# Kernel optimization log

Hardware: AMD Instinct MI355X
Metric: run time of the kernel (lower is better)

## Reference

```python
import jax, jax.numpy as jnp
import numpy as np

HEADS = 8
DIM_HEAD = 96
INNER = HEADS * DIM_HEAD  # 768
PEP_DIM = 768
PRO_DIM = 768
SCALE = DIM_HEAD ** -0.5
NEG = -1000000.0
EPS = 1e-5


def _layer_norm(x, g, b):
    mu = jnp.mean(x, axis=-1, keepdims=True)
    var = jnp.mean(jnp.square(x - mu), axis=-1, keepdims=True)
    return (x - mu) * jax.lax.rsqrt(var + EPS) * g + b


def setup_inputs() -> dict:
    key = jax.random.key(0)
    ks = jax.random.split(key, 12)
    b, n, m = 16, 128, 2048
    peptide = jax.random.normal(ks[0], (b, n, PEP_DIM), dtype=jnp.float32)
    protein = jax.random.normal(ks[1], (b, m, PRO_DIM), dtype=jnp.float32)
    peptide_mask = jax.random.randint(ks[2], (b, n), 0, 2, dtype=jnp.int32)
    pro_mask = jax.random.randint(ks[3], (b, m), 0, 2, dtype=jnp.int32)
    s = 0.02
    Wq = jax.random.normal(ks[4], (PEP_DIM, INNER), dtype=jnp.float32) * s
    Wk = jax.random.normal(ks[5], (PRO_DIM, INNER), dtype=jnp.float32) * s
    Wv_prot = jax.random.normal(ks[6], (PRO_DIM, INNER), dtype=jnp.float32) * s
    Wv_pep = jax.random.normal(ks[7], (PEP_DIM, INNER), dtype=jnp.float32) * s
    Wo_prot = jax.random.normal(ks[8], (INNER, PEP_DIM), dtype=jnp.float32) * s
    bo_prot = jnp.zeros((PEP_DIM,), dtype=jnp.float32)
    Wo_pep = jax.random.normal(ks[9], (INNER, PRO_DIM), dtype=jnp.float32) * s
    bo_pep = jnp.zeros((PRO_DIM,), dtype=jnp.float32)
    ln_g = jnp.ones((PEP_DIM,), dtype=jnp.float32)
    ln_b = jnp.zeros((PEP_DIM,), dtype=jnp.float32)
    return {
        'peptide': peptide, 'protein': protein,
        'peptide_mask': peptide_mask, 'pro_mask': pro_mask,
        'Wq': Wq, 'Wk': Wk, 'Wv_prot': Wv_prot, 'Wv_pep': Wv_pep,
        'Wo_prot': Wo_prot, 'bo_prot': bo_prot,
        'Wo_pep': Wo_pep, 'bo_pep': bo_pep,
        'ln_g': ln_g, 'ln_b': ln_b,
    }


def reference(peptide, protein, peptide_mask, pro_mask,
              Wq, Wk, Wv_prot, Wv_pep, Wo_prot, bo_prot, Wo_pep, bo_pep,
              ln_g, ln_b):
    b, n, _ = peptide.shape
    m = protein.shape[1]
    # projections -> (b, h, len, d)
    q = (peptide @ Wq).reshape(b, n, HEADS, DIM_HEAD).transpose(0, 2, 1, 3)
    k = (protein @ Wk).reshape(b, m, HEADS, DIM_HEAD).transpose(0, 2, 1, 3)
    v_prot = (protein @ Wv_prot).reshape(b, m, HEADS, DIM_HEAD).transpose(0, 2, 1, 3)
    v_pep = (peptide @ Wv_pep).reshape(b, n, HEADS, DIM_HEAD).transpose(0, 2, 1, 3)
    # scores (b, h, n, m)
    dots = jnp.einsum('bhnd,bhmd->bhnm', q, k) * SCALE
    dots = jnp.where(peptide_mask[:, None, :, None] == 0, NEG, dots)
    dots = jnp.where(pro_mask[:, None, None, :] == 0, NEG, dots)
    attn = jax.nn.softmax(dots, axis=-1)
    # peptide-side output: rows of attn aggregate protein values
    out_protein = jnp.einsum('bhnm,bhmd->bhnd', attn, v_prot)
    out_protein = out_protein.transpose(0, 2, 1, 3).reshape(b, n, INNER)
    out_protein = out_protein @ Wo_prot + bo_prot
    out_protein = _layer_norm(out_protein + peptide, ln_g, ln_b)
    # protein-side output: attn^T aggregates peptide values
    out_peptide = jnp.einsum('bhnm,bhnd->bhmd', attn, v_pep)
    out_peptide = out_peptide.transpose(0, 2, 1, 3).reshape(b, m, INNER)
    out_peptide = out_peptide @ Wo_pep + bo_pep
    out_peptide = _layer_norm(out_peptide + protein, ln_g, ln_b)
    return (out_protein, out_peptide, attn)
```

## Files before the change

### kernel.cpp

```cpp
#include <hip/hip_runtime.h>
#include <math.h>

static constexpr int HEADS  = 8;
static constexpr int DHEAD  = 96;
static constexpr int INNER  = 768;
static constexpr int NPEP   = 128;
static constexpr int MPRO   = 2048;
static constexpr float ATT_SCALE = 0.10206207261596577f;
static constexpr float NEGF   = -1000000.0f;
static constexpr float LN_EPS = 1e-5f;

typedef __attribute__((ext_vector_type(8))) short bf16x8;
typedef __attribute__((ext_vector_type(4))) float f32x4;

__device__ __forceinline__ unsigned short f2b(float f) {
    unsigned u = __builtin_bit_cast(unsigned, f);
    u += 0x7fffu + ((u >> 16) & 1u);
    return (unsigned short)(u >> 16);
}
__device__ __forceinline__ float b2f(unsigned short u) {
    return __builtin_bit_cast(float, (unsigned)u << 16);
}

__device__ __forceinline__ void async16(const unsigned short* g, unsigned short* l) {
    __builtin_amdgcn_global_load_lds(
        (const __attribute__((address_space(1))) void*)g,
        (__attribute__((address_space(3))) void*)l, 16, 0, 0);
}

template<int TM, int MODE>
__global__ __launch_bounds__(256) void gemm_bf16(
    const unsigned short* __restrict__ A, const unsigned short* __restrict__ B,
    unsigned short* __restrict__ C,
    int M, int N, int K, int lda, int ldb, int ldc,
    long sAb, long sAh, long sBb, long sBh, long sCb, long sCh,
    int lenShift, int nxSwz,
    const unsigned short* __restrict__ B2, unsigned short* __restrict__ C2)
{
    (void)M;
    constexpr int FR   = TM / 32;
    constexpr int PIPE = 3;
    __shared__ unsigned short As[PIPE][TM * 32];
    __shared__ unsigned short Bs[PIPE][128 * 32];

    const int tid = threadIdx.x;
    int bx, by;
    if (nxSwz > 0) {
        const int bid = blockIdx.x;
        const int per = gridDim.x >> 3;
        const int v   = (bid & 7) * per + (bid >> 3);
        bx = v % nxSwz; by = v / nxSwz;
    } else { bx = blockIdx.x; by = blockIdx.y; }
    int n0        = bx * 128;
    const int m0  = by * TM;
    const int z   = blockIdx.z;
    const int zb  = z >> 3, zh = z & 7;

    bool sideB = false;
    if (MODE == 5 && n0 >= 768) { sideB = true; n0 -= 768; }

    const unsigned short* Ab = A + zb * sAb + zh * sAh;
    const unsigned short* Bb = ((MODE == 5 && sideB) ? B2 : B) + zb * sBb + zh * sBh;

    const int rS = tid >> 2;
    const int kS = (((tid & 3) ^ ((rS >> 1) & 3)) * 8);
    const int wave = tid >> 6;

    const int lane = tid & 63;
    const int l16  = lane & 15;
    const int quad = lane >> 4;
    const int wr   = (wave >> 1) * (TM / 2);
    const int wc   = (wave & 1) * 64;

    f32x4 acc[FR][4];
#pragma unroll
    for (int i = 0; i < FR; ++i)
#pragma unroll
        for (int j = 0; j < 4; ++j) acc[i][j] = (f32x4){0.f, 0.f, 0.f, 0.f};

    auto stageT = [&](int t, int bi) {
        const int k0 = t << 5;
        unsigned short* a0 = &As[bi][wave * 512];
        async16(Ab + (long)(m0 + rS) * lda + k0 + kS, a0);
        if (TM == 128)
            async16(Ab + (long)(m0 + 64 + rS) * lda + k0 + kS, a0 + 2048);
        int bR0 = n0 + rS;      if (bR0 > N - 1) bR0 = N - 1;
        int bR1 = n0 + 64 + rS; if (bR1 > N - 1) bR1 = N - 1;
        unsigned short* b0 = &Bs[bi][wave * 512];
        async16(Bb + (long)bR0 * ldb + k0 + kS, b0);
        async16(Bb + (long)bR1 * ldb + k0 + kS, b0 + 2048);
    };

    const int NT = K >> 5;
    stageT(0, 0);
    if (NT > 1) stageT(1, 1);
    if (NT > 2) stageT(2, 2);

    int bi = 0;
    for (int t = 0; t < NT; ++t) {
        __syncthreads();

        bf16x8 af[FR], bfr[4];
#pragma unroll
        for (int i = 0; i < FR; ++i) {
            const int rA = wr + i * 16 + l16;
            af[i] = *reinterpret_cast<const bf16x8*>(
                &As[bi][rA * 32 + ((quad ^ ((rA >> 1) & 3)) * 8)]);
        }
#pragma unroll
        for (int j = 0; j < 4; ++j) {
            const int rB = wc + j * 16 + l16;
            bfr[j] = *reinterpret_cast<const bf16x8*>(
                &Bs[bi][rB * 32 + ((quad ^ ((rB >> 1) & 3)) * 8)]);
        }

#pragma unroll
        for (int i = 0; i < FR; ++i)
#pragma unroll
            for (int j = 0; j < 4; ++j)
                acc[i][j] = __builtin_amdgcn_mfma_f32_16x16x32_bf16(af[i], bfr[j], acc[i][j], 0, 0, 0);

        __syncthreads();
        if (t + PIPE < NT) stageT(t + PIPE, bi);
        bi = bi + 1; if (bi == PIPE) bi = 0;
    }

#pragma unroll
    for (int i = 0; i < FR; ++i) {
#pragma unroll
        for (int j = 0; j < 4; ++j) {
            const int col = n0 + wc + j * 16 + l16;
            if ((MODE == 2) && col >= N) continue;
            const int h = col / 96, d = col - h * 96;
#pragma unroll
            for (int r = 0; r < 4; ++r) {
                const int row = m0 + wr + i * 16 + quad * 4 + r;
                float v = acc[i][j][r];
                if (MODE == 1) {
                    v *= ATT_SCALE;
                    C[zb * sCb + zh * sCh + (long)row * ldc + col] = f2b(v);
                } else if (MODE == 2) {
                    C[zb * sCb + zh * sCh + (long)row * ldc + col] = f2b(v);
                } else if (MODE == 3) {
                    const int bb = row >> lenShift, rr = row & ((1 << lenShift) - 1);
                    C[(((long)(bb * 8 + h) << lenShift) + rr) * 96 + d] = f2b(v);
                } else if (MODE == 4) {
                    const int bb = row >> lenShift, rr = row & ((1 << lenShift) - 1);
                    C[(((long)(bb * 8 + h) * 96 + d) << lenShift) + rr] = f2b(v);
                } else {
                    const int bb = row >> lenShift, rr = row & ((1 << lenShift) - 1);
                    if (!sideB)
                        C [(((long)(bb * 8 + h) << lenShift) + rr) * 96 + d] = f2b(v);
                    else
                        C2[(((long)(bb * 8 + h) * 96 + d) << lenShift) + rr] = f2b(v);
                }
            }
        }
    }
}

__global__ __launch_bounds__(256) void fusedpv_kernel(
    const unsigned short* __restrict__ attn16,
    const unsigned short* __restrict__ vprotT,
    const unsigned short* __restrict__ vpepT,
    unsigned short* __restrict__ opp,
    unsigned short* __restrict__ opep)
{
    __shared__ unsigned short AttT[128 * 136];
    __shared__ unsigned short Vp[96 * 136];

    const int id = blockIdx.x;
    const int z  = ((id >> 4) << 3) + (id & 7);
    const int nh = (id >> 3) & 1;
    const int b  = z >> 3, h = z & 7;

    const unsigned short* Az = attn16 + (long)z * NPEP * MPRO;
    const unsigned short* Vz = vprotT + (long)z * 96 * MPRO;
    const unsigned short* Pz = vpepT  + (long)z * 96 * 128;

    const int tid  = threadIdx.x;
    const int lane = tid & 63;
    const int l16  = lane & 15;
    const int quad = lane >> 4;
    const int wave = tid >> 6;
    const int wrN  = (wave >> 1) * 32;
    const int wrM  = (wave >> 1) * 64;
    const int wcD  = (wave & 1) * 48;

#pragma unroll
    for (int e = 0; e < 6; ++e) {
        const int c = tid + e * 256;
        const int row = c >> 4, coloff = (c & 15) * 8;
        bf16x8 v = *reinterpret_cast<const bf16x8*>(Pz + row * 128 + coloff);
        *reinterpret_cast<bf16x8*>(&Vp[row * 136 + coloff]) = v;
    }
    __syncthreads();

    f32x4 acc1[2][3];
#pragma unroll
    for (int i = 0; i < 2; ++i)
#pragma unroll
        for (int j = 0; j < 3; ++j) acc1[i][j] = (f32x4){0.f, 0.f, 0.f, 0.f};

    for (int cc = 0; cc < 16; ++cc) {
        const int m0 = cc * 128;
        const bool own = (cc >> 3) == nh;

        bf16x8 a1[2][4], b1[3][4];
#pragma unroll
        for (int i = 0; i < 2; ++i) {
            const int n = nh * 64 + wrN + i * 16 + l16;
#pragma unroll
            for (int kc = 0; kc < 4; ++kc)
                a1[i][kc] = *reinterpret_cast<const bf16x8*>(
                    Az + (long)n * MPRO + m0 + kc * 32 + quad * 8);
        }
#pragma unroll
        for (int j = 0; j < 3; ++j) {
            const int d = wcD + j * 16 + l16;
#pragma unroll
            for (int kc = 0; kc < 4; ++kc)
                b1[j][kc] = *reinterpret_cast<const bf16x8*>(
                    Vz + (long)d * MPRO + m0 + kc * 32 + quad * 8);
        }

        if (own) {
            const int mBase = (tid & 7) * 16;
#pragma unroll
            for (int nn = 0; nn < 128; nn += 32) {
                const int n = nn + (tid >> 3);
#pragma unroll
                for (int c = 0; c < 2; ++c) {
                    bf16x8 v = *reinterpret_cast<const bf16x8*>(
                        Az + (long)n * MPRO + m0 + mBase + c * 8);
#pragma unroll
                    for (int jj = 0; jj < 8; ++jj)
                        AttT[(mBase + c * 8 + jj) * 136 + n] = (unsigned short)v[jj];
                }
            }
            __syncthreads();
        }

#pragma unroll
        for (int kc = 0; kc < 4; ++kc)
#pragma unroll
            for (int i = 0; i < 2; ++i)
#pragma unroll
                for (int j = 0; j < 3; ++j)
                    acc1[i][j] = __builtin_amdgcn_mfma_f32_16x16x32_bf16(
                        a1[i][kc], b1[j][kc], acc1[i][j], 0, 0, 0);

        if (own) {
            f32x4 acc2[4][3];
#pragma unroll
            for (int i = 0; i < 4; ++i)
#pragma unroll
                for (int j = 0; j < 3; ++j) acc2[i][j] = (f32x4){0.f, 0.f, 0.f, 0.f};
#pragma unroll
            for (int kc = 0; kc < 4; ++kc) {
                bf16x8 a2[4], b2v[3];
#pragma unroll
                for (int i = 0; i < 4; ++i)
                    a2[i] = *reinterpret_cast<const bf16x8*>(
                        &AttT[(wrM + i * 16 + l16) * 136 + kc * 32 + quad * 8]);
#pragma unroll
                for (int j = 0; j < 3; ++j)
                    b2v[j] = *reinterpret_cast<const bf16x8*>(
                        &Vp[(wcD + j * 16 + l16) * 136 + kc * 32 + quad * 8]);
#pragma unroll
                for (int i = 0; i < 4; ++i)
#pragma unroll
                    for (int j = 0; j < 3; ++j)
                        acc2[i][j] = __builtin_amdgcn_mfma_f32_16x16x32_bf16(
                            a2[i], b2v[j], acc2[i][j], 0, 0, 0);
            }
#pragma unroll
            for (int i = 0; i < 4; ++i)
#pragma unroll
                for (int j = 0; j < 3; ++j) {
                    const int d = wcD + j * 16 + l16;
#pragma unroll
                    for (int r = 0; r < 4; ++r) {
                        const int m = m0 + wrM + i * 16 + quad * 4 + r;
                        opep[(long)b * MPRO * INNER + (long)m * INNER + h * 96 + d]
                            = f2b(acc2[i][j][r]);
                    }
                }
            __syncthreads();
        }
    }

#pragma unroll
    for (int i = 0; i < 2; ++i)
#pragma unroll
        for (int j = 0; j < 3; ++j) {
            const int d = wcD + j * 16 + l16;
#pragma unroll
            for (int r = 0; r < 4; ++r) {
                const int n = nh * 64 + wrN + i * 16 + quad * 4 + r;
                opp[((long)b * NPEP + n) * INNER + h * 96 + d] = f2b(acc1[i][j][r]);
            }
        }
}

__global__ __launch_bounds__(256) void conv2_kernel(
    const float* __restrict__ pro, const float* __restrict__ pep,
    unsigned short* __restrict__ pro16, unsigned short* __restrict__ pep16,
    int nPro4, int nPep4)
{
    const int i = blockIdx.x * 256 + threadIdx.x;
    const float* in; unsigned short* out; int idx;
    if (i < nPro4) { in = pro; out = pro16; idx = i; }
    else { idx = i - nPro4; if (idx >= nPep4) return; in = pep; out = pep16; }
    float4 v = reinterpret_cast<const float4*>(in)[idx];
    ushort4 o;
    o.x = f2b(v.x); o.y = f2b(v.y); o.z = f2b(v.z); o.w = f2b(v.w);
    reinterpret_cast<ushort4*>(out)[idx] = o;
}

__global__ __launch_bounds__(256) void wtrans_kernel(
    const float* w0, const float* w1, const float* w2,
    const float* w3, const float* w4, const float* w5,
    unsigned short* o0, unsigned short* o1, unsigned short* o2,
    unsigned short* o3, unsigned short* o4, unsigned short* o5)
{
    const float* in; unsigned short* out;
    switch (blockIdx.z) {
        case 0: in = w0; out = o0; break;
        case 1: in = w1; out = o1; break;
        case 2: in = w2; out = o2; break;
        case 3: in = w3; out = o3; break;
        case 4: in = w4; out = o4; break;
        default: in = w5; out = o5; break;
    }
    __shared__ unsigned short t[32][33];
    const int bx = blockIdx.x * 32, by = blockIdx.y * 32;
    const int x = threadIdx.x, y = threadIdx.y;
#pragma unroll
    for (int i = 0; i < 32; i += 8)
        t[y + i][x] = f2b(in[(long)(by + y + i) * 768 + bx + x]);
    __syncthreads();
#pragma unroll
    for (int i = 0; i < 32; i += 8)
        out[(long)(bx + y + i) * 768 + by + x] = t[x][y + i];
}

__global__ __launch_bounds__(256) void softmax_kernel(
    unsigned short* __restrict__ s16, float* __restrict__ attn,
    const int* __restrict__ pepm, const int* __restrict__ prom)
{
    __shared__ float smx[4], sms[4];
    const long row = blockIdx.x;
    const int b = (int)(row >> 10);
    const int n = (int)(row & 127);
    unsigned short* p16 = s16 + row * (long)MPRO;
    float* pf = attn + row * (long)MPRO;
    const int tid = threadIdx.x;
    const int wv = tid >> 6;
    const int rowOk = pepm[(b << 7) + n];

    float v[8];
    float mx = -3.4e38f;
    if (rowOk) {
#pragma unroll
        for (int k = 0; k < 8; ++k) {
            const int c = tid + k * 256;
            float x = b2f(p16[c]);
            if (prom[(b << 11) + c] == 0) x = NEGF;
            v[k] = x; mx = fmaxf(mx, x);
        }
    } else {
#pragma unroll
        for (int k = 0; k < 8; ++k) v[k] = NEGF;
        mx = NEGF;
    }
#pragma unroll
    for (int off = 32; off > 0; off >>= 1) mx = fmaxf(mx, __shfl_xor(mx, off));
    if ((tid & 63) == 0) smx[wv] = mx;
    __syncthreads();
    mx = fmaxf(fmaxf(smx[0], smx[1]), fmaxf(smx[2], smx[3]));

    float sum = 0.f;
#pragma unroll
    for (int k = 0; k < 8; ++k) { v[k] = __expf(v[k] - mx); sum += v[k]; }
#pragma unroll
    for (int off = 32; off > 0; off >>= 1) sum += __shfl_xor(sum, off);
    if ((tid & 63) == 0) sms[wv] = sum;
    __syncthreads();
    const float inv = 1.0f / (sms[0] + sms[1] + sms[2] + sms[3]);
#pragma unroll
    for (int k = 0; k < 8; ++k) {
        const float o = v[k] * inv;
        pf[tid + k * 256] = o;
        p16[tid + k * 256] = f2b(o);
    }
}

__global__ __launch_bounds__(256) void bias_res_ln(
    const unsigned short* __restrict__ tmp, const float* __restrict__ bias,
    const float* __restrict__ res, const float* __restrict__ gam,
    const float* __restrict__ bet, float* __restrict__ out)
{
    __shared__ float red[8];
    const long row = blockIdx.x;
    const unsigned short* t = tmp + row * INNER;
    const float* r = res + row * INNER;
    float* o = out + row * INNER;
    const int tid = threadIdx.x;
    const int wv = tid >> 6;

    float v[3]; float s = 0.f;
#pragma unroll
    for (int k = 0; k < 3; ++k) { const int c = tid + k * 256; v[k] = b2f(t[c]) + bias[c] + r[c]; s += v[k]; }
#pragma unroll
    for (int off = 32; off > 0; off >>= 1) s += __shfl_xor(s, off);
    if ((tid & 63) == 0) red[wv] = s;
    __syncthreads();
    const float mu = (red[0] + red[1] + red[2] + red[3]) * (1.0f / INNER);

    float vs = 0.f;
#pragma unroll
    for (int k = 0; k < 3; ++k) { const float d = v[k] - mu; vs += d * d; }
#pragma unroll
    for (int off = 32; off > 0; off >>= 1) vs += __shfl_xor(vs, off);
    if ((tid & 63) == 0) red[4 + wv] = vs;
    __syncthreads();
    const float rstd = rsqrtf((red[4] + red[5] + red[6] + red[7]) * (1.0f / INNER) + LN_EPS);
#pragma unroll
    for (int k = 0; k < 3; ++k) { const int c = tid + k * 256; o[c] = (v[k] - mu) * rstd * gam[c] + bet[c]; }
}

extern "C" void kernel_launch(void* const* d_in, const int* in_sizes, int n_in,
                              void* d_out, int out_size, void* d_ws, size_t ws_size,
                              hipStream_t stream)
{
    (void)in_sizes; (void)n_in; (void)out_size; (void)ws_size;

    const float* peptide = (const float*)d_in[0];
    const float* protein = (const float*)d_in[1];
    const int*   pepm    = (const int*)  d_in[2];
    const int*   prom    = (const int*)  d_in[3];
    const float* Wq      = (const float*)d_in[4];
    const float* Wk      = (const float*)d_in[5];
    const float* Wv_prot = (const float*)d_in[6];
    const float* Wv_pep  = (const float*)d_in[7];
    const float* Wo_prot = (const float*)d_in[8];
    const float* bo_prot = (const float*)d_in[9];
    const float* Wo_pep  = (const float*)d_in[10];
    const float* bo_pep  = (const float*)d_in[11];
    const float* ln_g    = (const float*)d_in[12];
    const float* ln_b    = (const float*)d_in[13];

    char* ws = (char*)d_ws;
    auto U = [&](size_t off) { return (unsigned short*)(ws + off); };
    unsigned short* WT0   = U(0);
    unsigned short* WT1   = U(1179648);
    unsigned short* WT2   = U(2 * 1179648);
    unsigned short* WT3   = U(3 * 1179648);
    unsigned short* WT4   = U(4 * 1179648);
    unsigned short* WT5   = U(5 * 1179648);
    unsigned short* q16   = U(7077888);
    unsigned short* k16   = U(10223616);
    unsigned short* vpT   = U(60555264);
    unsigned short* vpepT = U(110886912);
    unsigned short* s16   = U(114032640);
    unsigned short* pro16 = U(114032640);
    unsigned short* pep16 = U(164364288);
    unsigned short* opp   = U(7077888);
    unsigned short* opep  = U(10223616);
    unsigned short* tmp1  = U(164364288);
    unsigned short* tmp2  = U(63700992);

    float* outP = (float*)d_out;
    float* outQ = outP + 16 * 128 * 768;
    float* attn = outQ + (long)16 * 2048 * 768;

    conv2_kernel<<<26112, 256, 0, stream>>>(protein, peptide, pro16, pep16, 6291456, 393216);
    wtrans_kernel<<<dim3(24, 24, 6), dim3(32, 8), 0, stream>>>(
        Wq, Wk, Wv_prot, Wv_pep, Wo_prot, Wo_pep, WT0, WT1, WT2, WT3, WT4, WT5);

    gemm_bf16<128, 5><<<dim3(12, 16, 1), 256, 0, stream>>>(
        pep16, WT0, q16, 2048, 768, 768, 768, 768, 0,
        0, 0, 0, 0, 0, 0, 7, 0, WT3, vpepT);
    gemm_bf16<128, 5><<<dim3(3072, 1, 1), 256, 0, stream>>>(
        pro16, WT1, k16, 32768, 768, 768, 768, 768, 0,
        0, 0, 0, 0, 0, 0, 11, 12, WT2, vpT);

    gemm_bf16<128, 1><<<dim3(16, 1, 128), 256, 0, stream>>>(
        q16, k16, s16, 128, 2048, 96, 96, 96, 2048,
        98304L, 12288L, 1572864L, 196608L, 2097152L, 262144L, 0, 0, nullptr, nullptr);

    softmax_kernel<<<16384, 256, 0, stream>>>(s16, attn, pepm, prom);

    fusedpv_kernel<<<256, 256, 0, stream>>>(s16, vpT, vpepT, opp, opep);

    gemm_bf16<64, 2><<<dim3(6, 32, 1), 256, 0, stream>>>(
        opp, WT4, tmp1, 2048, 768, 768, 768, 768, 768,
        0, 0, 0, 0, 0, 0, 0, 0, nullptr, nullptr);
    bias_res_ln<<<2048, 256, 0, stream>>>(tmp1, bo_prot, peptide, ln_g, ln_b, outP);

    gemm_bf16<128, 2><<<dim3(1536, 1, 1), 256, 0, stream>>>(
        opep, WT5, tmp2, 32768, 768, 768, 768, 768, 768,
        0, 0, 0, 0, 0, 0, 0, 6, nullptr, nullptr);
    bias_res_ln<<<32768, 256, 0, stream>>>(tmp2, bo_pep, protein, ln_g, ln_b, outQ);
}
```

Before: 768.1 us.

## Replace LDS-staged GEMM with direct-to-register global loads and double buffering

The GEMM kernel no longer stages A/B tiles through shared memory with async global-to-LDS loads and a 3-stage pipeline. Each lane now loads its MFMA fragments straight from global memory into registers, ping-ponging two register buffers so the next K step's loads overlap the current MFMAs. This removes LDS traffic and the per-step barriers. In exchange, operands are no longer shared within the workgroup, so each wave re-reads from global/L2 with narrower, less coalesced 16-byte accesses. Unused store modes and the unused M parameter are also dropped.

```diff
diff --git a/kernel.cpp b/kernel.cpp
--- a/kernel.cpp
+++ b/kernel.cpp
@@ -22,34 +22,23 @@
     return __builtin_bit_cast(float, (unsigned)u << 16);
 }
 
-__device__ __forceinline__ void async16(const unsigned short* g, unsigned short* l) {
-    __builtin_amdgcn_global_load_lds(
-        (const __attribute__((address_space(1))) void*)g,
-        (__attribute__((address_space(3))) void*)l, 16, 0, 0);
-}
-
 template<int TM, int MODE>
-__global__ __launch_bounds__(256) void gemm_bf16(
+__global__ __launch_bounds__(256) void gemm_dg(
     const unsigned short* __restrict__ A, const unsigned short* __restrict__ B,
     unsigned short* __restrict__ C,
-    int M, int N, int K, int lda, int ldb, int ldc,
+    int N, int K, int lda, int ldb, int ldc,
     long sAb, long sAh, long sBb, long sBh, long sCb, long sCh,
-    int lenShift, int nxSwz,
+    int lenShift, int nx,
     const unsigned short* __restrict__ B2, unsigned short* __restrict__ C2)
 {
-    (void)M;
-    constexpr int FR   = TM / 32;
-    constexpr int PIPE = 3;
-    __shared__ unsigned short As[PIPE][TM * 32];
-    __shared__ unsigned short Bs[PIPE][128 * 32];
-
+    constexpr int FR = TM / 32;
     const int tid = threadIdx.x;
     int bx, by;
-    if (nxSwz > 0) {
+    if (nx > 0) {
         const int bid = blockIdx.x;
         const int per = gridDim.x >> 3;
         const int v   = (bid & 7) * per + (bid >> 3);
-        bx = v % nxSwz; by = v / nxSwz;
+        bx = v % nx; by = v / nx;
     } else { bx = blockIdx.x; by = blockIdx.y; }
     int n0        = bx * 128;
     const int m0  = by * TM;
@@ -62,68 +51,59 @@
     const unsigned short* Ab = A + zb * sAb + zh * sAh;
     const unsigned short* Bb = ((MODE == 5 && sideB) ? B2 : B) + zb * sBb + zh * sBh;
 
-    const int rS = tid >> 2;
-    const int kS = (((tid & 3) ^ ((rS >> 1) & 3)) * 8);
     const int wave = tid >> 6;
-
     const int lane = tid & 63;
     const int l16  = lane & 15;
     const int quad = lane >> 4;
     const int wr   = (wave >> 1) * (TM / 2);
     const int wc   = (wave & 1) * 64;
 
+    const unsigned short* pA[FR];
+    const unsigned short* pB[4];
+#pragma unroll
+    for (int i = 0; i < FR; ++i)
+        pA[i] = Ab + (long)(m0 + wr + i * 16 + l16) * lda + quad * 8;
+#pragma unroll
+    for (int j = 0; j < 4; ++j) {
+        int br = n0 + wc + j * 16 + l16; if (br > N - 1) br = N - 1;
+        pB[j] = Bb + (long)br * ldb + quad * 8;
+    }
+
     f32x4 acc[FR][4];
 #pragma unroll
     for (int i = 0; i < FR; ++i)
 #pragma unroll
         for (int j = 0; j < 4; ++j) acc[i][j] = (f32x4){0.f, 0.f, 0.f, 0.f};
 
-    auto stageT = [&](int t, int bi) {
-        const int k0 = t << 5;
-        unsigned short* a0 = &As[bi][wave * 512];
-        async16(Ab + (long)(m0 + rS) * lda + k0 + kS, a0);
-        if (TM == 128)
-            async16(Ab + (long)(m0 + 64 + rS) * lda + k0 + kS, a0 + 2048);
-        int bR0 = n0 + rS;      if (bR0 > N - 1) bR0 = N - 1;
-        int bR1 = n0 + 64 + rS; if (bR1 > N - 1) bR1 = N - 1;
-        unsigned short* b0 = &Bs[bi][wave * 512];
-        async16(Bb + (long)bR0 * ldb + k0 + kS, b0);
-        async16(Bb + (long)bR1 * ldb + k0 + kS, b0 + 2048);
+    bf16x8 afA[FR], bfA[4], afB[FR], bfB[4];
+
+    auto LOAD = [&](bf16x8* af, bf16x8* bf, int t) {
+        const int k = t * 32;
+#pragma unroll
+        for (int i = 0; i < FR; ++i)
+            af[i] = *reinterpret_cast<const bf16x8*>(pA[i] + k);
+#pragma unroll
+        for (int j = 0; j < 4; ++j)
+            bf[j] = *reinterpret_cast<const bf16x8*>(pB[j] + k);
     };
+    auto STEP = [&](const bf16x8* af, const bf16x8* bf) {
+#pragma unroll
+        for (int i = 0; i < FR; ++i)
+#pragma unroll
+            for (int j = 0; j < 4; ++j)
+                acc[i][j] = __builtin_amdgcn_mfma_f32_16x16x32_bf16(af[i], bf[j], acc[i][j], 0, 0, 0);
+    };
 
     const int NT = K >> 5;
-    stageT(0, 0);
-    if (NT > 1) stageT(1, 1);
-    if (NT > 2) stageT(2, 2);
-
-    int bi = 0;
-    for (int t = 0; t < NT; ++t) {
-        __syncthreads();
-
-        bf16x8 af[FR], bfr[4];
-#pragma unroll
-        for (int i = 0; i < FR; ++i) {
-            const int rA = wr + i * 16 + l16;
-            af[i] = *reinterpret_cast<const bf16x8*>(
-                &As[bi][rA * 32 + ((quad ^ ((rA >> 1) & 3)) * 8)]);
-        }
-#pragma unroll
-        for (int j = 0; j < 4; ++j) {
-            const int rB = wc + j * 16 + l16;
-            bfr[j] = *reinterpret_cast<const bf16x8*>(
-                &Bs[bi][rB * 32 + ((quad ^ ((rB >> 1) & 3)) * 8)]);
-        }
-
-#pragma unroll
-        for (int i = 0; i < FR; ++i)
-#pragma unroll
-            for (int j = 0; j < 4; ++j)
-                acc[i][j] = __builtin_amdgcn_mfma_f32_16x16x32_bf16(af[i], bfr[j], acc[i][j], 0, 0, 0);
-
-        __syncthreads();
-        if (t + PIPE < NT) stageT(t + PIPE, bi);
-        bi = bi + 1; if (bi == PIPE) bi = 0;
-    }
+    LOAD(afA, bfA, 0);
+    int t = 0;
+    for (; t + 2 <= NT; t += 2) {
+        if (t + 1 < NT) LOAD(afB, bfB, t + 1);
+        STEP(afA, bfA);
+        if (t + 2 < NT) LOAD(afA, bfA, t + 2);
+        STEP(afB, bfB);
+    }
+    if (t < NT) STEP(afA, bfA);
 
 #pragma unroll
     for (int i = 0; i < FR; ++i) {
@@ -141,12 +121,6 @@
                     C[zb * sCb + zh * sCh + (long)row * ldc + col] = f2b(v);
                 } else if (MODE == 2) {
                     C[zb * sCb + zh * sCh + (long)row * ldc + col] = f2b(v);
-                } else if (MODE == 3) {
-                    const int bb = row >> lenShift, rr = row & ((1 << lenShift) - 1);
-                    C[(((long)(bb * 8 + h) << lenShift) + rr) * 96 + d] = f2b(v);
-                } else if (MODE == 4) {
-                    const int bb = row >> lenShift, rr = row & ((1 << lenShift) - 1);
-                    C[(((long)(bb * 8 + h) * 96 + d) << lenShift) + rr] = f2b(v);
                 } else {
                     const int bb = row >> lenShift, rr = row & ((1 << lenShift) - 1);
                     if (!sideB)
@@ -479,28 +453,28 @@
     wtrans_kernel<<<dim3(24, 24, 6), dim3(32, 8), 0, stream>>>(
         Wq, Wk, Wv_prot, Wv_pep, Wo_prot, Wo_pep, WT0, WT1, WT2, WT3, WT4, WT5);
 
-    gemm_bf16<128, 5><<<dim3(12, 16, 1), 256, 0, stream>>>(
-        pep16, WT0, q16, 2048, 768, 768, 768, 768, 0,
+    gemm_dg<128, 5><<<dim3(12, 16, 1), 256, 0, stream>>>(
+        pep16, WT0, q16, 768, 768, 768, 768, 0,
         0, 0, 0, 0, 0, 0, 7, 0, WT3, vpepT);
-    gemm_bf16<128, 5><<<dim3(3072, 1, 1), 256, 0, stream>>>(
-        pro16, WT1, k16, 32768, 768, 768, 768, 768, 0,
+    gemm_dg<128, 5><<<dim3(3072, 1, 1), 256, 0, stream>>>(
+        pro16, WT1, k16, 768, 768, 768, 768, 0,
         0, 0, 0, 0, 0, 0, 11, 12, WT2, vpT);
 
-    gemm_bf16<128, 1><<<dim3(16, 1, 128), 256, 0, stream>>>(
-        q16, k16, s16, 128, 2048, 96, 96, 96, 2048,
+    gemm_dg<128, 1><<<dim3(16, 1, 128), 256, 0, stream>>>(
+        q16, k16, s16, 2048, 96, 96, 96, 2048,
         98304L, 12288L, 1572864L, 196608L, 2097152L, 262144L, 0, 0, nullptr, nullptr);
 
     softmax_kernel<<<16384, 256, 0, stream>>>(s16, attn, pepm, prom);
 
     fusedpv_kernel<<<256, 256, 0, stream>>>(s16, vpT, vpepT, opp, opep);
 
-    gemm_bf16<64, 2><<<dim3(6, 32, 1), 256, 0, stream>>>(
-        opp, WT4, tmp1, 2048, 768, 768, 768, 768, 768,
+    gemm_dg<64, 2><<<dim3(6, 32, 1), 256, 0, stream>>>(
+        opp, WT4, tmp1, 768, 768, 768, 768, 768,
         0, 0, 0, 0, 0, 0, 0, 0, nullptr, nullptr);
     bias_res_ln<<<2048, 256, 0, stream>>>(tmp1, bo_prot, peptide, ln_g, ln_b, outP);
 
-    gemm_bf16<128, 2><<<dim3(1536, 1, 1), 256, 0, stream>>>(
-        opep, WT5, tmp2, 32768, 768, 768, 768, 768, 768,
+    gemm_dg<128, 2><<<dim3(1536, 1, 1), 256, 0, stream>>>(
+        opep, WT5, tmp2, 768, 768, 768, 768, 768,
         0, 0, 0, 0, 0, 0, 0, 6, nullptr, nullptr);
     bias_res_ln<<<32768, 256, 0, stream>>>(tmp2, bo_pep, protein, ln_g, ln_b, outQ);
 }
```

After: 1.013 ms. 1.32x slower.
